# Performance work log

Hardware: AMD Instinct MI355X
Metric: run time of the kernel (lower is better)

The kernel has to match this reference:

```python
import jax, jax.numpy as jnp
import numpy as np

B, T = 32, 4096
QD, MD, AD = 1024, 512, 128
F, K = 32, 31
PAD = (K - 1) // 2  # 'same' padding as in Tacotron-2 location conv


def setup_inputs() -> dict:
    key = jax.random.key(0)
    ks = jax.random.split(key, 12)
    s = lambda fan_in: 1.0 / np.sqrt(fan_in)
    return {
        "query": jax.random.normal(ks[0], (B, QD), jnp.float32),
        "memory": jax.random.normal(ks[1], (B, T, MD), jnp.float32),
        "alignments": jax.random.uniform(ks[2], (B, T, 2), jnp.float32),
        "mask": jnp.zeros((B, T), dtype=bool),
        "Wq": jax.random.normal(ks[3], (QD, AD), jnp.float32) * s(QD),
        "bq": jnp.zeros((AD,), jnp.float32),
        "Wm": jax.random.normal(ks[4], (MD, AD), jnp.float32) * s(MD),
        "bm": jnp.zeros((AD,), jnp.float32),
        "conv_w": jax.random.normal(ks[5], (F, 2, K), jnp.float32) * s(2 * K),
        "conv_b": jnp.zeros((F,), jnp.float32),
        "Wl": jax.random.normal(ks[6], (F, AD), jnp.float32) * s(F),
        "bl": jnp.zeros((AD,), jnp.float32),
        "v_w": jax.random.normal(ks[7], (AD,), jnp.float32) * s(AD),
        "v_b": jnp.zeros((), jnp.float32),
    }


def reference(query, memory, alignments, mask, Wq, bq, Wm, bm, conv_w, conv_b, Wl, bl, v_w, v_b):
    # processed memory: [B, T, AD]
    processed_memory = jnp.einsum("btm,ma->bta", memory, Wm) + bm
    # processed query: [B, 1, AD] (query.unsqueeze(1))
    processed_query = (query @ Wq + bq)[:, None, :]
    # location features: conv over time on [B, 2, T] -> [B, F, T]
    a = jnp.transpose(alignments, (0, 2, 1))  # [B, 2, T]
    loc = jax.lax.conv_general_dilated(
        a, conv_w, window_strides=(1,), padding=[(PAD, PAD)],
        dimension_numbers=("NCH", "OIH", "NCH"))
    loc = loc + conv_b[None, :, None]
    loc = jnp.transpose(loc, (0, 2, 1))  # [B, T, F]
    processed_loc = jnp.einsum("btf,fa->bta", loc, Wl) + bl
    # additive score: v . tanh(q + m + l)  -> [B, T]
    score = jnp.einsum("bta,a->bt", jnp.tanh(processed_query + processed_memory + processed_loc), v_w) + v_b
    score = jnp.where(mask, -jnp.inf, score)
    alignment = jax.nn.softmax(score, axis=-1)  # [B, T]
    context = jnp.einsum("bt,btm->bm", alignment, memory)  # [B, MD]
    return context, alignment
```

## Files before the change

kernel.cpp:

```cpp
#include <hip/hip_runtime.h>
#include <hip/hip_bf16.h>
#include <math.h>

#define B_ 32
#define T_ 4096
#define QD_ 1024
#define MD_ 512
#define AD_ 128
#define F_ 32
#define K_ 31
#define PAD_ 15

#define TT 64

typedef float f32x16 __attribute__((ext_vector_type(16)));
typedef unsigned int uint4v __attribute__((ext_vector_type(4)));

__device__ inline unsigned pk_bf2(float lo, float hi) {
    unsigned ul = __float_as_uint(lo) + 0x8000u;
    unsigned uh = __float_as_uint(hi) + 0x8000u;
    return __builtin_amdgcn_perm(uh, ul, 0x07060302u);
}

__device__ inline unsigned short f2bf_rn(float f) {
    unsigned u = __float_as_uint(f);
    u += 0x7fffu + ((u >> 16) & 1u);
    return (unsigned short)(u >> 16);
}

__device__ inline void mfma32(f32x16& c, uint4v a, uint4v b) {
    asm("s_nop 1\n\tv_mfma_f32_32x32x16_bf16 %0, %1, %2, %0"
        : "+v"(c) : "v"(a), "v"(b));
}

__global__ __launch_bounds__(256) void k_prep(const float* __restrict__ Wm,
                                              unsigned short* __restrict__ wmT) {
    int i = blockIdx.x * 256 + threadIdx.x;
    int k = i & (MD_ - 1);
    int a = i >> 9;
    wmT[i] = f2bf_rn(Wm[k * AD_ + a]);
}

__global__ __launch_bounds__(128) void k_pq(const float* __restrict__ query,
                                            const float* __restrict__ Wq,
                                            float* __restrict__ pq) {
    int b = blockIdx.x;
    int qc = blockIdx.y;
    int a = threadIdx.x;
    const float* qrow = query + b * QD_ + qc * 128;
    const float* wq = Wq + (qc * 128) * AD_ + a;
    float acc = 0.f;
#pragma unroll 4
    for (int i = 0; i < 128; i++) acc += qrow[i] * wq[i * AD_];
    atomicAdd(&pq[b * AD_ + a], acc);
}

__global__ __launch_bounds__(256) void k_score(
    const float* __restrict__ memory, const float* __restrict__ alignments,
    const unsigned char* __restrict__ mask,
    const unsigned short* __restrict__ wmT, const float* __restrict__ bm,
    const float* __restrict__ convw, const float* __restrict__ convb,
    const float* __restrict__ Wl, const float* __restrict__ bl,
    const float* __restrict__ vw, const float* __restrict__ vb,
    const float* __restrict__ pq, const float* __restrict__ bq,
    float* __restrict__ scores) {
    __shared__ float s_base[TT * AD_];
    __shared__ float s_convw[F_ * 2 * K_];
    __shared__ float s_align[(TT + K_ - 1) * 2];
    __shared__ float s_loc[TT * F_];
    __shared__ float s_score[TT];

    const int tid = threadIdx.x;
    const int b = blockIdx.y;
    const int t0 = blockIdx.x * TT;

    if (tid < TT) s_score[tid] = 0.f;

    for (int i = tid; i < F_ * 2 * K_; i += 256) s_convw[i] = convw[i];
    for (int i = tid; i < (TT + K_ - 1) * 2; i += 256) {
        int tg = t0 + (i >> 1) - PAD_;
        s_align[i] = (tg >= 0 && tg < T_) ? alignments[((long)b * T_ + tg) * 2 + (i & 1)] : 0.f;
    }
    __syncthreads();

    for (int i = tid; i < TT * F_; i += 256) {
        int f = i & (F_ - 1);
        int t = i >> 5;
        float acc = convb[f];
        const float* w0 = &s_convw[f * (2 * K_)];
        const float* w1 = w0 + K_;
        const float* al = &s_align[t * 2];
#pragma unroll
        for (int k = 0; k < K_; k++) {
            acc += al[2 * k] * w0[k] + al[2 * k + 1] * w1[k];
        }
        s_loc[t * F_ + f] = acc;
    }
    __syncthreads();

    for (int i = tid; i < TT * AD_; i += 256) {
        int a = i & (AD_ - 1);
        int t = i >> 7;
        float acc = pq[b * AD_ + a] + bq[a] + bm[a] + bl[a];
        const float* lrow = &s_loc[t * F_];
#pragma unroll
        for (int f = 0; f < F_; f++) acc += lrow[f] * Wl[f * AD_ + a];
        s_base[i] = acc;
    }
    __syncthreads();

    const int lane = tid & 63;
    const int w = tid >> 6;
    const int rt = w >> 1;
    const int ct0 = (w & 1) * 2;
    const int half = lane >> 5;
    const int l31 = lane & 31;

    const float* arow = memory + ((long)(b * T_ + t0 + rt * 32 + l31)) * MD_ + half * 8;
    const unsigned short* wb0 = wmT + (ct0 * 32 + l31) * MD_ + half * 8;
    const unsigned short* wb1 = wb0 + 32 * MD_;

    f32x16 c0, c1;
#pragma unroll
    for (int i = 0; i < 16; i++) { c0[i] = 0.f; c1[i] = 0.f; }

#pragma unroll 4
    for (int k0 = 0; k0 < MD_; k0 += 16) {
        float4 a0 = *(const float4*)(arow + k0);
        float4 a1 = *(const float4*)(arow + k0 + 4);
        uint4v bf0 = *(const uint4v*)(wb0 + k0);
        uint4v bf1 = *(const uint4v*)(wb1 + k0);
        uint4v af;
        af[0] = pk_bf2(a0.x, a0.y);
        af[1] = pk_bf2(a0.z, a0.w);
        af[2] = pk_bf2(a1.x, a1.y);
        af[3] = pk_bf2(a1.z, a1.w);
        mfma32(c0, af, bf0);
        mfma32(c1, af, bf1);
    }
    asm volatile("s_nop 7\n\ts_nop 7\n\ts_nop 7" ::: "memory");

    float vwa0 = vw[ct0 * 32 + l31];
    float vwa1 = vw[ct0 * 32 + 32 + l31];
#pragma unroll
    for (int i = 0; i < 16; i++) {
        int t = rt * 32 + (i & 3) + 8 * (i >> 2) + 4 * half;
        float v0 = tanhf(c0[i] + s_base[t * AD_ + ct0 * 32 + l31]) * vwa0;
        float v1 = tanhf(c1[i] + s_base[t * AD_ + ct0 * 32 + 32 + l31]) * vwa1;
        float s = v0 + v1;
        s += __shfl_xor(s, 1);
        s += __shfl_xor(s, 2);
        s += __shfl_xor(s, 4);
        s += __shfl_xor(s, 8);
        s += __shfl_xor(s, 16);
        if (l31 == 0) atomicAdd(&s_score[t], s);
    }
    __syncthreads();

    if (tid < TT) {
        int tg = t0 + tid;
        float val = s_score[tid] + vb[0];
        if (mask[(long)b * T_ + tg]) val = -INFINITY;
        scores[b * T_ + tg] = val;
    }
}

__global__ __launch_bounds__(256) void k_softmax(const float* __restrict__ scores,
                                                 float* __restrict__ oalign) {
    int b = blockIdx.x;
    int tid = threadIdx.x;
    __shared__ float red[4];
    __shared__ float s_max, s_sum;

    float m = -INFINITY;
    for (int t = tid; t < T_; t += 256) m = fmaxf(m, scores[b * T_ + t]);
    for (int off = 32; off >= 1; off >>= 1) m = fmaxf(m, __shfl_xor(m, off));
    if ((tid & 63) == 0) red[tid >> 6] = m;
    __syncthreads();
    if (tid == 0) {
        float mm = red[0];
        for (int i = 1; i < 4; i++) mm = fmaxf(mm, red[i]);
        s_max = mm;
    }
    __syncthreads();
    float mm = s_max;

    float sum = 0.f;
    for (int t = tid; t < T_; t += 256) sum += expf(scores[b * T_ + t] - mm);
    for (int off = 32; off >= 1; off >>= 1) sum += __shfl_xor(sum, off);
    if ((tid & 63) == 0) red[tid >> 6] = sum;
    __syncthreads();
    if (tid == 0) {
        float ss = 0.f;
        for (int i = 0; i < 4; i++) ss += red[i];
        s_sum = ss;
    }
    __syncthreads();
    float inv = 1.f / s_sum;
    for (int t = tid; t < T_; t += 256) {
        oalign[b * T_ + t] = expf(scores[b * T_ + t] - mm) * inv;
    }
}

__global__ __launch_bounds__(256) void k_context(const float* __restrict__ oalign,
                                                 const float* __restrict__ memory,
                                                 float* __restrict__ ctx) {
    int b = blockIdx.x;
    int md = blockIdx.y * 256 + threadIdx.x;
    int tc = blockIdx.z * 512;
    __shared__ float s_a[512];
    for (int i = threadIdx.x; i < 512; i += 256) s_a[i] = oalign[b * T_ + tc + i];
    __syncthreads();
    float acc = 0.f;
    const float* mp = memory + ((long)b * T_ + tc) * MD_ + md;
#pragma unroll 4
    for (int t = 0; t < 512; t++) acc += s_a[t] * mp[(long)t * MD_];
    atomicAdd(&ctx[b * MD_ + md], acc);
}

extern "C" void kernel_launch(void* const* d_in, const int* in_sizes, int n_in,
                              void* d_out, int out_size, void* d_ws, size_t ws_size,
                              hipStream_t stream) {
    const float* query      = (const float*)d_in[0];
    const float* memory     = (const float*)d_in[1];
    const float* alignments = (const float*)d_in[2];
    const unsigned char* mask = (const unsigned char*)d_in[3];
    const float* Wq    = (const float*)d_in[4];
    const float* bq    = (const float*)d_in[5];
    const float* Wm    = (const float*)d_in[6];
    const float* bm    = (const float*)d_in[7];
    const float* convw = (const float*)d_in[8];
    const float* convb = (const float*)d_in[9];
    const float* Wl    = (const float*)d_in[10];
    const float* bl    = (const float*)d_in[11];
    const float* vw    = (const float*)d_in[12];
    const float* vb    = (const float*)d_in[13];

    float* out = (float*)d_out;
    float* ctx = out;
    float* oalign = out + B_ * MD_;

    float* ws = (float*)d_ws;
    float* pq = ws;
    float* scores = ws + B_ * AD_;
    unsigned short* wmT = (unsigned short*)(ws + B_ * AD_ + B_ * T_);

    hipMemsetAsync(pq, 0, B_ * AD_ * sizeof(float), stream);
    hipMemsetAsync(ctx, 0, B_ * MD_ * sizeof(float), stream);

    k_prep<<<(AD_ * MD_) / 256, 256, 0, stream>>>(Wm, wmT);
    k_pq<<<dim3(B_, QD_ / 128), 128, 0, stream>>>(query, Wq, pq);
    k_score<<<dim3(T_ / TT, B_), 256, 0, stream>>>(
        memory, alignments, mask, wmT, bm, convw, convb, Wl, bl, vw, vb, pq, bq, scores);
    k_softmax<<<B_, 256, 0, stream>>>(scores, oalign);
    k_context<<<dim3(B_, MD_ / 256, T_ / 512), 256, 0, stream>>>(oalign, memory, ctx);
}
```

Before: 550.7 us.

## Fuse context into score kernel with blockwise online softmax and LDS-staged MFMA

The score kernel now computes per-block softmax partials (local max, denominator) and a weighted partial context over its 64 timesteps, while the memory tile is still cache-resident. A small reduce kernel then rescales and combines them, replacing the separate softmax and context kernels and their second full read of memory. The MFMA A operand is staged through double-buffered LDS with prefetch, and Wm is pre-swizzled into MFMA fragment order. s_base is stored as bf16 to cut LDS use and allow four blocks per CU, at some precision risk.

```diff
diff --git a/kernel.cpp b/kernel.cpp
--- a/kernel.cpp
+++ b/kernel.cpp
@@ -12,6 +12,7 @@
 #define PAD_ 15
 
 #define TT 64
+#define NBLK (T_ / TT)
 
 typedef float f32x16 __attribute__((ext_vector_type(16)));
 typedef unsigned int uint4v __attribute__((ext_vector_type(4)));
@@ -28,17 +29,32 @@
     return (unsigned short)(u >> 16);
 }
 
+__device__ inline float bf2f(unsigned short u) {
+    return __uint_as_float(((unsigned)u) << 16);
+}
+
 __device__ inline void mfma32(f32x16& c, uint4v a, uint4v b) {
     asm("s_nop 1\n\tv_mfma_f32_32x32x16_bf16 %0, %1, %2, %0"
         : "+v"(c) : "v"(a), "v"(b));
 }
 
 __global__ __launch_bounds__(256) void k_prep(const float* __restrict__ Wm,
-                                              unsigned short* __restrict__ wmT) {
-    int i = blockIdx.x * 256 + threadIdx.x;
-    int k = i & (MD_ - 1);
-    int a = i >> 9;
-    wmT[i] = f2bf_rn(Wm[k * AD_ + a]);
+                                              unsigned short* __restrict__ wmT_sw) {
+    int gid = blockIdx.x * 256 + threadIdx.x;
+    int kk = gid >> 8;
+    int ct = (gid >> 6) & 3;
+    int lane = gid & 63;
+    int k0 = kk * 16 + (lane >> 5) * 8;
+    int a = ct * 32 + (lane & 31);
+    unsigned short o[8];
+#pragma unroll
+    for (int j = 0; j < 8; j++) o[j] = f2bf_rn(Wm[(k0 + j) * AD_ + a]);
+    uint4v v;
+    v[0] = ((unsigned)o[1] << 16) | o[0];
+    v[1] = ((unsigned)o[3] << 16) | o[2];
+    v[2] = ((unsigned)o[5] << 16) | o[4];
+    v[3] = ((unsigned)o[7] << 16) | o[6];
+    *(uint4v*)(wmT_sw + (long)gid * 8) = v;
 }
 
 __global__ __launch_bounds__(128) void k_pq(const float* __restrict__ query,
@@ -55,31 +71,37 @@
     atomicAdd(&pq[b * AD_ + a], acc);
 }
 
-__global__ __launch_bounds__(256) void k_score(
+__global__ __launch_bounds__(256, 4) void k_score_ctx(
     const float* __restrict__ memory, const float* __restrict__ alignments,
     const unsigned char* __restrict__ mask,
-    const unsigned short* __restrict__ wmT, const float* __restrict__ bm,
+    const unsigned short* __restrict__ wmT_sw, const float* __restrict__ bm,
     const float* __restrict__ convw, const float* __restrict__ convb,
     const float* __restrict__ Wl, const float* __restrict__ bl,
     const float* __restrict__ vw, const float* __restrict__ vb,
     const float* __restrict__ pq, const float* __restrict__ bq,
-    float* __restrict__ scores) {
-    __shared__ float s_base[TT * AD_];
-    __shared__ float s_convw[F_ * 2 * K_];
-    __shared__ float s_align[(TT + K_ - 1) * 2];
-    __shared__ float s_loc[TT * F_];
+    float* __restrict__ scores, float* __restrict__ bmax,
+    float* __restrict__ bden, float* __restrict__ num) {
+    __shared__ __align__(16) unsigned short s_base[TT * AD_];
+    __shared__ __align__(16) unsigned char s_u[16896];
     __shared__ float s_score[TT];
+    __shared__ float s_w[TT];
 
     const int tid = threadIdx.x;
     const int b = blockIdx.y;
-    const int t0 = blockIdx.x * TT;
+    const int blk = blockIdx.x;
+    const int t0 = blk * TT;
+
+    float* convw_s = (float*)s_u;
+    float* align_s = convw_s + 1984;
+    float* loc_s   = align_s + 192;
+    unsigned short* sab = (unsigned short*)s_u;
 
     if (tid < TT) s_score[tid] = 0.f;
 
-    for (int i = tid; i < F_ * 2 * K_; i += 256) s_convw[i] = convw[i];
+    for (int i = tid; i < F_ * 2 * K_; i += 256) convw_s[i] = convw[i];
     for (int i = tid; i < (TT + K_ - 1) * 2; i += 256) {
         int tg = t0 + (i >> 1) - PAD_;
-        s_align[i] = (tg >= 0 && tg < T_) ? alignments[((long)b * T_ + tg) * 2 + (i & 1)] : 0.f;
+        align_s[i] = (tg >= 0 && tg < T_) ? alignments[((long)b * T_ + tg) * 2 + (i & 1)] : 0.f;
     }
     __syncthreads();
 
@@ -87,14 +109,12 @@
         int f = i & (F_ - 1);
         int t = i >> 5;
         float acc = convb[f];
-        const float* w0 = &s_convw[f * (2 * K_)];
+        const float* w0 = &convw_s[f * (2 * K_)];
         const float* w1 = w0 + K_;
-        const float* al = &s_align[t * 2];
-#pragma unroll
-        for (int k = 0; k < K_; k++) {
-            acc += al[2 * k] * w0[k] + al[2 * k + 1] * w1[k];
-        }
-        s_loc[t * F_ + f] = acc;
+        const float* al = &align_s[t * 2];
+#pragma unroll
+        for (int k = 0; k < K_; k++) acc += al[2 * k] * w0[k] + al[2 * k + 1] * w1[k];
+        loc_s[t * F_ + f] = acc;
     }
     __syncthreads();
 
@@ -102,10 +122,10 @@
         int a = i & (AD_ - 1);
         int t = i >> 7;
         float acc = pq[b * AD_ + a] + bq[a] + bm[a] + bl[a];
-        const float* lrow = &s_loc[t * F_];
+        const float* lrow = &loc_s[t * F_];
 #pragma unroll
         for (int f = 0; f < F_; f++) acc += lrow[f] * Wl[f * AD_ + a];
-        s_base[i] = acc;
+        s_base[i] = f2bf_rn(acc);
     }
     __syncthreads();
 
@@ -116,27 +136,62 @@
     const int half = lane >> 5;
     const int l31 = lane & 31;
 
-    const float* arow = memory + ((long)(b * T_ + t0 + rt * 32 + l31)) * MD_ + half * 8;
-    const unsigned short* wb0 = wmT + (ct0 * 32 + l31) * MD_ + half * 8;
-    const unsigned short* wb1 = wb0 + 32 * MD_;
+    const int srow = tid >> 3;
+    const int skq = (tid & 7) * 4;
+    const float* aptr = memory + ((long)b * T_ + t0) * MD_;
+    const float* g_lo = aptr + srow * MD_ + skq;
+    const float* g_hi = aptr + (srow + 32) * MD_ + skq;
+    unsigned short* w_lo[2], * w_hi[2];
+    w_lo[0] = sab + srow * 40 + skq;          w_hi[0] = sab + (srow + 32) * 40 + skq;
+    w_lo[1] = w_lo[0] + 2560;                 w_hi[1] = w_hi[0] + 2560;
+
+    const unsigned short* bptr = wmT_sw + ((long)ct0 * 64 + lane) * 8;
+    const int arow = (rt * 32 + l31) * 40 + half * 8;
 
     f32x16 c0, c1;
 #pragma unroll
     for (int i = 0; i < 16; i++) { c0[i] = 0.f; c1[i] = 0.f; }
 
-#pragma unroll 4
-    for (int k0 = 0; k0 < MD_; k0 += 16) {
-        float4 a0 = *(const float4*)(arow + k0);
-        float4 a1 = *(const float4*)(arow + k0 + 4);
-        uint4v bf0 = *(const uint4v*)(wb0 + k0);
-        uint4v bf1 = *(const uint4v*)(wb1 + k0);
-        uint4v af;
-        af[0] = pk_bf2(a0.x, a0.y);
-        af[1] = pk_bf2(a0.z, a0.w);
-        af[2] = pk_bf2(a1.x, a1.y);
-        af[3] = pk_bf2(a1.z, a1.w);
-        mfma32(c0, af, bf0);
-        mfma32(c1, af, bf1);
+    float4 A0 = *(const float4*)(g_lo);
+    float4 A1 = *(const float4*)(g_hi);
+    uint4v B00 = *(const uint4v*)(bptr);
+    uint4v B01 = *(const uint4v*)(bptr + 512);
+    uint4v B10 = *(const uint4v*)(bptr + 2048);
+    uint4v B11 = *(const uint4v*)(bptr + 2048 + 512);
+    ((unsigned*)w_lo[0])[0] = pk_bf2(A0.x, A0.y);
+    ((unsigned*)w_lo[0])[1] = pk_bf2(A0.z, A0.w);
+    ((unsigned*)w_hi[0])[0] = pk_bf2(A1.x, A1.y);
+    ((unsigned*)w_hi[0])[1] = pk_bf2(A1.z, A1.w);
+    __syncthreads();
+
+    for (int c = 0; c < 16; c++) {
+        const int cb = c & 1, nb = cb ^ 1;
+        float4 N0, N1;
+        uint4v NB00, NB01, NB10, NB11;
+        {
+            int kcn = (c < 15) ? (c + 1) * 32 : 0;
+            N0 = *(const float4*)(g_lo + kcn);
+            N1 = *(const float4*)(g_hi + kcn);
+            long kkn = (c < 15) ? (long)(2 * c + 2) * 2048 : 0;
+            NB00 = *(const uint4v*)(bptr + kkn);
+            NB01 = *(const uint4v*)(bptr + kkn + 512);
+            NB10 = *(const uint4v*)(bptr + kkn + 2048);
+            NB11 = *(const uint4v*)(bptr + kkn + 2048 + 512);
+        }
+        uint4v af0 = *(const uint4v*)(sab + cb * 2560 + arow);
+        uint4v af1 = *(const uint4v*)(sab + cb * 2560 + arow + 16);
+        mfma32(c0, af0, B00);
+        mfma32(c1, af0, B01);
+        mfma32(c0, af1, B10);
+        mfma32(c1, af1, B11);
+        B00 = NB00; B01 = NB01; B10 = NB10; B11 = NB11;
+        if (c < 15) {
+            ((unsigned*)w_lo[nb])[0] = pk_bf2(N0.x, N0.y);
+            ((unsigned*)w_lo[nb])[1] = pk_bf2(N0.z, N0.w);
+            ((unsigned*)w_hi[nb])[0] = pk_bf2(N1.x, N1.y);
+            ((unsigned*)w_hi[nb])[1] = pk_bf2(N1.z, N1.w);
+        }
+        __syncthreads();
     }
     asm volatile("s_nop 7\n\ts_nop 7\n\ts_nop 7" ::: "memory");
 
@@ -145,9 +200,9 @@
 #pragma unroll
     for (int i = 0; i < 16; i++) {
         int t = rt * 32 + (i & 3) + 8 * (i >> 2) + 4 * half;
-        float v0 = tanhf(c0[i] + s_base[t * AD_ + ct0 * 32 + l31]) * vwa0;
-        float v1 = tanhf(c1[i] + s_base[t * AD_ + ct0 * 32 + 32 + l31]) * vwa1;
-        float s = v0 + v1;
+        float b0 = bf2f(s_base[t * AD_ + ct0 * 32 + l31]);
+        float b1 = bf2f(s_base[t * AD_ + ct0 * 32 + 32 + l31]);
+        float s = tanhf(c0[i] + b0) * vwa0 + tanhf(c1[i] + b1) * vwa1;
         s += __shfl_xor(s, 1);
         s += __shfl_xor(s, 2);
         s += __shfl_xor(s, 4);
@@ -158,64 +213,73 @@
     __syncthreads();
 
     if (tid < TT) {
-        int tg = t0 + tid;
-        float val = s_score[tid] + vb[0];
-        if (mask[(long)b * T_ + tg]) val = -INFINITY;
-        scores[b * T_ + tg] = val;
-    }
-}
-
-__global__ __launch_bounds__(256) void k_softmax(const float* __restrict__ scores,
-                                                 float* __restrict__ oalign) {
+        float s = s_score[tid] + vb[0];
+        bool mk = mask[(long)b * T_ + t0 + tid] != 0;
+        if (mk) s = -INFINITY;
+        scores[b * T_ + t0 + tid] = s;
+        float m = s;
+#pragma unroll
+        for (int off = 32; off >= 1; off >>= 1) m = fmaxf(m, __shfl_xor(m, off));
+        float e = (m == -INFINITY) ? 0.f : expf(s - m);
+        float d = e;
+#pragma unroll
+        for (int off = 32; off >= 1; off >>= 1) d += __shfl_xor(d, off);
+        s_w[tid] = e;
+        if (tid == 0) {
+            bmax[b * NBLK + blk] = m;
+            bden[b * NBLK + blk] = d;
+        }
+    }
+    __syncthreads();
+
+    {
+        const float2* mp = (const float2*)aptr + tid;
+        float ax = 0.f, ay = 0.f;
+#pragma unroll 8
+        for (int t = 0; t < TT; t++) {
+            float2 v = mp[t * 256];
+            float wt = s_w[t];
+            ax += wt * v.x;
+            ay += wt * v.y;
+        }
+        float2 o; o.x = ax; o.y = ay;
+        *(float2*)(num + ((long)b * NBLK + blk) * MD_ + tid * 2) = o;
+    }
+}
+
+__global__ __launch_bounds__(512) void k_reduce(
+    const float* __restrict__ bmax, const float* __restrict__ bden,
+    const float* __restrict__ num, const float* __restrict__ scores,
+    float* __restrict__ ctx, float* __restrict__ oalign) {
     int b = blockIdx.x;
     int tid = threadIdx.x;
-    __shared__ float red[4];
-    __shared__ float s_max, s_sum;
-
-    float m = -INFINITY;
-    for (int t = tid; t < T_; t += 256) m = fmaxf(m, scores[b * T_ + t]);
-    for (int off = 32; off >= 1; off >>= 1) m = fmaxf(m, __shfl_xor(m, off));
-    if ((tid & 63) == 0) red[tid >> 6] = m;
+    __shared__ float sm[NBLK], se[NBLK];
+    __shared__ float sD;
+    if (tid < NBLK) sm[tid] = bmax[b * NBLK + tid];
+    __syncthreads();
+    float M = -INFINITY;
+#pragma unroll
+    for (int i = 0; i < NBLK; i++) M = fmaxf(M, sm[i]);
+    if (tid < NBLK) se[tid] = expf(sm[tid] - M) * bden[b * NBLK + tid];
     __syncthreads();
     if (tid == 0) {
-        float mm = red[0];
-        for (int i = 1; i < 4; i++) mm = fmaxf(mm, red[i]);
-        s_max = mm;
-    }
-    __syncthreads();
-    float mm = s_max;
-
-    float sum = 0.f;
-    for (int t = tid; t < T_; t += 256) sum += expf(scores[b * T_ + t] - mm);
-    for (int off = 32; off >= 1; off >>= 1) sum += __shfl_xor(sum, off);
-    if ((tid & 63) == 0) red[tid >> 6] = sum;
-    __syncthreads();
-    if (tid == 0) {
-        float ss = 0.f;
-        for (int i = 0; i < 4; i++) ss += red[i];
-        s_sum = ss;
-    }
-    __syncthreads();
-    float inv = 1.f / s_sum;
-    for (int t = tid; t < T_; t += 256) {
-        oalign[b * T_ + t] = expf(scores[b * T_ + t] - mm) * inv;
-    }
-}
-
-__global__ __launch_bounds__(256) void k_context(const float* __restrict__ oalign,
-                                                 const float* __restrict__ memory,
-                                                 float* __restrict__ ctx) {
-    int b = blockIdx.x;
-    int md = blockIdx.y * 256 + threadIdx.x;
-    int tc = blockIdx.z * 512;
-    __shared__ float s_a[512];
-    for (int i = threadIdx.x; i < 512; i += 256) s_a[i] = oalign[b * T_ + tc + i];
-    __syncthreads();
+        float D = 0.f;
+        for (int i = 0; i < NBLK; i++) D += se[i];
+        sD = D;
+    }
+    if (tid < NBLK) se[tid] = expf(sm[tid] - M);
+    __syncthreads();
+    float invD = 1.f / sD;
+
     float acc = 0.f;
-    const float* mp = memory + ((long)b * T_ + tc) * MD_ + md;
-#pragma unroll 4
-    for (int t = 0; t < 512; t++) acc += s_a[t] * mp[(long)t * MD_];
-    atomicAdd(&ctx[b * MD_ + md], acc);
+    const float* np = num + (long)b * NBLK * MD_ + tid;
+#pragma unroll 8
+    for (int blk = 0; blk < NBLK; blk++) acc += se[blk] * np[blk * MD_];
+    ctx[b * MD_ + tid] = acc * invD;
+
+    for (int t = tid; t < T_; t += 512) {
+        oalign[b * T_ + t] = expf(scores[b * T_ + t] - M) * invD;
+    }
 }
 
 extern "C" void kernel_launch(void* const* d_in, const int* in_sizes, int n_in,
@@ -241,17 +305,19 @@
     float* oalign = out + B_ * MD_;
 
     float* ws = (float*)d_ws;
-    float* pq = ws;
-    float* scores = ws + B_ * AD_;
-    unsigned short* wmT = (unsigned short*)(ws + B_ * AD_ + B_ * T_);
+    float* pq     = ws;
+    float* scores = pq + B_ * AD_;
+    float* bmax   = scores + B_ * T_;
+    float* bden   = bmax + B_ * NBLK;
+    float* num    = bden + B_ * NBLK;
+    unsigned short* wmT_sw = (unsigned short*)(num + (long)B_ * NBLK * MD_);
 
     hipMemsetAsync(pq, 0, B_ * AD_ * sizeof(float), stream);
-    hipMemsetAsync(ctx, 0, B_ * MD_ * sizeof(float), stream);
-
-    k_prep<<<(AD_ * MD_) / 256, 256, 0, stream>>>(Wm, wmT);
+
+    k_prep<<<32, 256, 0, stream>>>(Wm, wmT_sw);
     k_pq<<<dim3(B_, QD_ / 128), 128, 0, stream>>>(query, Wq, pq);
-    k_score<<<dim3(T_ / TT, B_), 256, 0, stream>>>(
-        memory, alignments, mask, wmT, bm, convw, convb, Wl, bl, vw, vb, pq, bq, scores);
-    k_softmax<<<B_, 256, 0, stream>>>(scores, oalign);
-    k_context<<<dim3(B_, MD_ / 256, T_ / 512), 256, 0, stream>>>(oalign, memory, ctx);
-}
+    k_score_ctx<<<dim3(NBLK, B_), 256, 0, stream>>>(
+        memory, alignments, mask, wmT_sw, bm, convw, convb, Wl, bl, vw, vb, pq, bq,
+        scores, bmax, bden, num);
+    k_reduce<<<B_, 512, 0, stream>>>(bmax, bden, num, scores, ctx, oalign);
+}
```

Measured after the change: 485.5 us. 11.8% less time.
